# Performance work log

Hardware: AMD Instinct MI355X
Metric: run time of the kernel (lower is better)

## Reference

```python
import jax, jax.numpy as jnp
import numpy as np


def setup_inputs() -> dict:
    key = jax.random.key(0)
    ks = jax.random.split(key, 6)
    Q, S, D, C = 128, 512, 768, 64
    return {
        "query_reps": jax.random.normal(ks[0], (Q, D), dtype=jnp.float32),
        "support_reps": jax.random.normal(ks[1], (S, D), dtype=jnp.float32),
        "W1": jax.random.normal(ks[2], (2 * D, 2 * D), dtype=jnp.float32) * 0.02,
        "b1": jnp.zeros((2 * D,), dtype=jnp.float32),
        "W2": jax.random.normal(ks[3], (1, 2 * D), dtype=jnp.float32) * 0.02,
        "b2": jnp.zeros((1,), dtype=jnp.float32),
        "support_labels": jnp.sort(jax.random.randint(ks[4], (S,), 0, C)),
        "query_target_ids": jax.random.randint(ks[5], (Q,), 0, C),
        "num_classes": C,
    }


def reference(query_reps, support_reps, W1, b1, W2, b2,
              support_labels, query_target_ids, num_classes):
    D = query_reps.shape[1]
    # Original: concat_reps = cat([repeat_interleave(q, S), s.repeat(Q)], dim=1)
    # then relu(Linear_2Dx2D(concat)). Equivalent split-weight form avoids the
    # explicit [Q*S, 2D] concat: x @ W1.T = q @ W1[:, :D].T + s @ W1[:, D:].T
    hq = query_reps @ W1[:, :D].T        # [Q, 2D]
    hs = support_reps @ W1[:, D:].T      # [S, 2D]
    h = jax.nn.relu(hq[:, None, :] + hs[None, :, :] + b1)   # [Q, S, 2D]
    scores = jnp.einsum('qsd,d->qs', h, W2[0]) + b2[0]       # [Q, S]
    # aggregate_scores_by_label with support_reduction='score':
    # M one-hot [C, S] row-normalized (p=1) => per-label mean of scores.
    seg = jax.ops.segment_sum(scores.T, support_labels,
                              num_segments=num_classes).T     # [Q, C]
    counts = jax.ops.segment_sum(jnp.ones((support_labels.shape[0],), jnp.float32),
                                 support_labels, num_segments=num_classes)
    agg = seg / jnp.maximum(counts, 1.0)                      # [Q, C]
    logp = jax.nn.log_softmax(agg, axis=1)
    loss = -jnp.mean(jnp.take_along_axis(logp, query_target_ids[:, None], axis=1))
    preds = jnp.argmax(agg, axis=1)
    return (loss, preds == query_target_ids)
```

## Files before the change

kernel.cpp:

```cpp
#include <hip/hip_runtime.h>
#include <math.h>

#define QN 128
#define SN 512
#define DN 768
#define TDN 1536
#define CN 64
#define KSPLIT 2
#define KCH 384

#define HQP_ELEMS (KSPLIT * QN * TDN)
#define HSP_ELEMS (KSPLIT * SN * TDN)
#define ZERO_ELEMS (QN * CN)

typedef short short8 __attribute__((ext_vector_type(8)));
typedef float f32x4 __attribute__((ext_vector_type(4)));

#define LDS_STRIDE 40
#define PLANE (128 * LDS_STRIDE)

__device__ __forceinline__ short bf16_rtn(float x) {
    unsigned u = __float_as_uint(x);
    return (short)((u + 0x7fffu + ((u >> 16) & 1u)) >> 16);
}
__device__ __forceinline__ float bf16_tof(short s) {
    return __uint_as_float(((unsigned)(unsigned short)s) << 16);
}

__global__ __launch_bounds__(256) void gemm_kernel(
    const float* __restrict__ query, const float* __restrict__ support,
    const float* __restrict__ W1, float* __restrict__ hqp, float* __restrict__ hsp,
    float* __restrict__ zbuf, float* __restrict__ out)
{
    const int nt = blockIdx.x;
    const int mt = blockIdx.y;
    const int kz = blockIdx.z;
    const int tid = threadIdx.x;

    if (nt == 0 && kz == 0) {
        int o = (mt * 256 + tid) * 8;
        if (o < ZERO_ELEMS) {
            *(float4*)&zbuf[o]     = make_float4(0.f, 0.f, 0.f, 0.f);
            *(float4*)&zbuf[o + 4] = make_float4(0.f, 0.f, 0.f, 0.f);
        }
        if (mt == 0 && tid == 0) out[0] = 0.0f;
    }

    const float* A;
    float* Cout;
    int M0, Koff;
    if (mt == 0) { A = query;   M0 = 0;              Koff = 0;  Cout = hqp + (size_t)kz * QN * TDN; }
    else         { A = support; M0 = (mt - 1) * 128; Koff = DN; Cout = hsp + (size_t)kz * SN * TDN; }

    __shared__ short lds[2][4][PLANE];

    const int r  = tid >> 1;
    const int kh = (tid & 1) * 16;

    const float* Arow = &A [(size_t)(M0 + r) * DN  + kz * KCH + kh];
    const float* Brow = &W1[(size_t)(nt * 128 + r) * TDN + Koff + kz * KCH + kh];

    f32x4 acc[4][4];
    #pragma unroll
    for (int i = 0; i < 4; ++i)
        #pragma unroll
        for (int j = 0; j < 4; ++j)
            acc[i][j] = (f32x4){0.f, 0.f, 0.f, 0.f};

    auto stage = [&](short* plane, float4 v0, float4 v1, float4 v2, float4 v3) {
        float f[16] = {v0.x,v0.y,v0.z,v0.w, v1.x,v1.y,v1.z,v1.w,
                       v2.x,v2.y,v2.z,v2.w, v3.x,v3.y,v3.z,v3.w};
        short hi[16], lo[16];
        #pragma unroll
        for (int i = 0; i < 16; ++i) {
            hi[i] = bf16_rtn(f[i]);
            lo[i] = bf16_rtn(f[i] - bf16_tof(hi[i]));
        }
        short* dsth = plane + r * LDS_STRIDE + kh;
        #pragma unroll
        for (int i = 0; i < 16; ++i) dsth[i] = hi[i];
        short* dstl = plane + PLANE + r * LDS_STRIDE + kh;
        #pragma unroll
        for (int i = 0; i < 16; ++i) dstl[i] = lo[i];
    };

    {
        float4 a0 = *(const float4*)(Arow),     a1 = *(const float4*)(Arow + 4);
        float4 a2 = *(const float4*)(Arow + 8), a3 = *(const float4*)(Arow + 12);
        float4 b0 = *(const float4*)(Brow),     b1 = *(const float4*)(Brow + 4);
        float4 b2 = *(const float4*)(Brow + 8), b3 = *(const float4*)(Brow + 12);
        stage(lds[0][0], a0, a1, a2, a3);
        stage(lds[0][2], b0, b1, b2, b3);
    }
    __syncthreads();

    const int lane  = tid & 63;
    const int w     = tid >> 6;
    const int lm    = lane & 15;
    const int quad  = lane >> 4;
    const int wrow0 = (w >> 1) * 64;
    const int wcol0 = (w & 1) * 64;

    int buf = 0;
    for (int step = 0; step < 12; ++step) {
        float4 a0, a1, a2, a3, b0, b1, b2, b3;
        if (step < 11) {
            const float* An = Arow + (step + 1) * 32;
            const float* Bn = Brow + (step + 1) * 32;
            a0 = *(const float4*)(An);     a1 = *(const float4*)(An + 4);
            a2 = *(const float4*)(An + 8); a3 = *(const float4*)(An + 12);
            b0 = *(const float4*)(Bn);     b1 = *(const float4*)(Bn + 4);
            b2 = *(const float4*)(Bn + 8); b3 = *(const float4*)(Bn + 12);
        }

        const short* Ah = lds[buf][0];
        const short* Al = lds[buf][1];
        const short* Bh = lds[buf][2];
        const short* Bl = lds[buf][3];

        short8 ah[4], al[4], bh[4], bl[4];
        #pragma unroll
        for (int mi = 0; mi < 4; ++mi) {
            int off = (wrow0 + mi * 16 + lm) * LDS_STRIDE + quad * 8;
            ah[mi] = *(const short8*)&Ah[off];
            al[mi] = *(const short8*)&Al[off];
        }
        #pragma unroll
        for (int ni = 0; ni < 4; ++ni) {
            int off = (wcol0 + ni * 16 + lm) * LDS_STRIDE + quad * 8;
            bh[ni] = *(const short8*)&Bh[off];
            bl[ni] = *(const short8*)&Bl[off];
        }
        #pragma unroll
        for (int mi = 0; mi < 4; ++mi)
            #pragma unroll
            for (int ni = 0; ni < 4; ++ni) {
                acc[mi][ni] = __builtin_amdgcn_mfma_f32_16x16x32_bf16(ah[mi], bh[ni], acc[mi][ni], 0, 0, 0);
                acc[mi][ni] = __builtin_amdgcn_mfma_f32_16x16x32_bf16(ah[mi], bl[ni], acc[mi][ni], 0, 0, 0);
                acc[mi][ni] = __builtin_amdgcn_mfma_f32_16x16x32_bf16(al[mi], bh[ni], acc[mi][ni], 0, 0, 0);
            }

        if (step < 11) {
            int nb = buf ^ 1;
            stage(lds[nb][0], a0, a1, a2, a3);
            stage(lds[nb][2], b0, b1, b2, b3);
            __syncthreads();
            buf = nb;
        }
    }

    #pragma unroll
    for (int mi = 0; mi < 4; ++mi)
        #pragma unroll
        for (int ni = 0; ni < 4; ++ni) {
            int grow = M0 + wrow0 + mi * 16 + quad * 4;
            int gcol = nt * 128 + wcol0 + ni * 16 + lm;
            #pragma unroll
            for (int rr = 0; rr < 4; ++rr)
                Cout[(size_t)(grow + rr) * TDN + gcol] = acc[mi][ni][rr];
        }
}

#define JC 48
#define SSTR 68

__global__ __launch_bounds__(256) void score_kernel(
    const float* __restrict__ hqp, const float* __restrict__ hsp,
    const float* __restrict__ b1, const float* __restrict__ W2,
    const int* __restrict__ labels, float* __restrict__ aggbuf)
{
    const int jc = blockIdx.x;
    const int qt = blockIdx.y;
    const int st = blockIdx.z;

    __shared__ float hqL[64 * SSTR];
    __shared__ float hsL[64 * SSTR];
    __shared__ float w2s[JC];
    __shared__ int   lab[64];

    const int tid = threadIdx.x;
    if (tid < 64) lab[tid] = labels[st * 64 + tid];
    if (tid < 12) *(float4*)&w2s[tid * 4] = *(const float4*)&W2[jc * JC + tid * 4];

    #pragma unroll
    for (int l = 0; l < 6; ++l) {
        int idx  = tid + l * 256;
        int isHS = idx >= 768;
        int slot = isHS ? idx - 768 : idx;
        int row  = slot / 12;
        int q4   = slot - row * 12;
        int j    = jc * JC + q4 * 4;
        int phys = q4 ^ ((row >> 2) & 7);
        if (!isHS) {
            float4 h0 = *(const float4*)&hqp[(size_t)(qt * 64 + row) * TDN + j];
            float4 h1 = *(const float4*)&hqp[(size_t)QN * TDN + (size_t)(qt * 64 + row) * TDN + j];
            float4 bb = *(const float4*)&b1[j];
            *(float4*)&hqL[row * SSTR + phys * 4] =
                make_float4(h0.x + h1.x + bb.x, h0.y + h1.y + bb.y,
                            h0.z + h1.z + bb.z, h0.w + h1.w + bb.w);
        } else {
            float4 g0 = *(const float4*)&hsp[(size_t)(st * 64 + row) * TDN + j];
            float4 g1 = *(const float4*)&hsp[(size_t)SN * TDN + (size_t)(st * 64 + row) * TDN + j];
            *(float4*)&hsL[row * SSTR + phys * 4] =
                make_float4(g0.x + g1.x, g0.y + g1.y, g0.z + g1.z, g0.w + g1.w);
        }
    }
    __syncthreads();

    const int tx = tid & 15;
    const int ty = tid >> 4;
    float acc[4][4];
    #pragma unroll
    for (int i = 0; i < 4; ++i)
        #pragma unroll
        for (int j = 0; j < 4; ++j) acc[i][j] = 0.0f;

    const int akey = ty & 7;
    const int bkey = tx & 7;

    for (int jj4 = 0; jj4 < 12; ++jj4) {
        float4 a4[4], b4[4];
        const int pa = (jj4 ^ akey) * 4;
        const int pb = (jj4 ^ bkey) * 4;
        #pragma unroll
        for (int i = 0; i < 4; ++i)
            a4[i] = *(const float4*)&hqL[(ty * 4 + i) * SSTR + pa];
        #pragma unroll
        for (int j = 0; j < 4; ++j)
            b4[j] = *(const float4*)&hsL[(tx * 4 + j) * SSTR + pb];
        float4 w4 = *(const float4*)&w2s[jj4 * 4];

        #pragma unroll
        for (int c = 0; c < 4; ++c) {
            float w = (c == 0) ? w4.x : (c == 1) ? w4.y : (c == 2) ? w4.z : w4.w;
            float a[4] = { (c==0)?a4[0].x:(c==1)?a4[0].y:(c==2)?a4[0].z:a4[0].w,
                           (c==0)?a4[1].x:(c==1)?a4[1].y:(c==2)?a4[1].z:a4[1].w,
                           (c==0)?a4[2].x:(c==1)?a4[2].y:(c==2)?a4[2].z:a4[2].w,
                           (c==0)?a4[3].x:(c==1)?a4[3].y:(c==2)?a4[3].z:a4[3].w };
            float b[4] = { (c==0)?b4[0].x:(c==1)?b4[0].y:(c==2)?b4[0].z:b4[0].w,
                           (c==0)?b4[1].x:(c==1)?b4[1].y:(c==2)?b4[1].z:b4[1].w,
                           (c==0)?b4[2].x:(c==1)?b4[2].y:(c==2)?b4[2].z:b4[2].w,
                           (c==0)?b4[3].x:(c==1)?b4[3].y:(c==2)?b4[3].z:b4[3].w };
            #pragma unroll
            for (int i = 0; i < 4; ++i)
                #pragma unroll
                for (int j = 0; j < 4; ++j)
                    acc[i][j] += w * fmaxf(a[i] + b[j], 0.0f);
        }
    }

    {
        const int l0 = lab[tx * 4 + 0], l1 = lab[tx * 4 + 1];
        const int l2 = lab[tx * 4 + 2], l3 = lab[tx * 4 + 3];
        #pragma unroll
        for (int i = 0; i < 4; ++i) {
            float* aggrow = aggbuf + (size_t)(qt * 64 + ty * 4 + i) * CN;
            float runv = acc[i][0];
            int   runc = l0;
            if (l1 != runc) { atomicAdd(&aggrow[runc], runv); runv = 0.0f; runc = l1; }
            runv += acc[i][1];
            if (l2 != runc) { atomicAdd(&aggrow[runc], runv); runv = 0.0f; runc = l2; }
            runv += acc[i][2];
            if (l3 != runc) { atomicAdd(&aggrow[runc], runv); runv = 0.0f; runc = l3; }
            runv += acc[i][3];
            atomicAdd(&aggrow[runc], runv);
        }
    }
}

__global__ __launch_bounds__(256) void finale_kernel(
    const float* __restrict__ aggbuf, const int* __restrict__ labels,
    const int* __restrict__ tgt, float* __restrict__ out)
{
    __shared__ float cnt[CN];
    const int tid = threadIdx.x;
    if (tid < CN) cnt[tid] = 0.0f;
    __syncthreads();
    atomicAdd(&cnt[labels[tid]],       1.0f);
    atomicAdd(&cnt[labels[tid + 256]], 1.0f);
    __syncthreads();

    const int lane = tid & 63;
    const int q    = blockIdx.x * 4 + (tid >> 6);

    float v = aggbuf[(size_t)q * CN + lane] / fmaxf(cnt[lane], 1.0f);
    float av = v; int am = lane;
    #pragma unroll
    for (int off = 1; off < 64; off <<= 1) {
        float ov = __shfl_xor(av, off);
        int   oi = __shfl_xor(am, off);
        if (ov > av || (ov == av && oi < am)) { av = ov; am = oi; }
    }
    float m = av;
    float e = expf(v - m);
    #pragma unroll
    for (int off = 1; off < 64; off <<= 1)
        e += __shfl_xor(e, off);
    int t = tgt[q];
    float vt = __shfl(v, t, 64);
    if (lane == 0) {
        out[1 + q] = (am == t) ? 1.0f : 0.0f;
        atomicAdd(&out[0], -(vt - m - logf(e)) / (float)QN);
    }
}

extern "C" void kernel_launch(void* const* d_in, const int* in_sizes, int n_in,
                              void* d_out, int out_size, void* d_ws, size_t ws_size,
                              hipStream_t stream) {
    const float* query   = (const float*)d_in[0];
    const float* support = (const float*)d_in[1];
    const float* W1      = (const float*)d_in[2];
    const float* b1      = (const float*)d_in[3];
    const float* W2      = (const float*)d_in[4];
    const int* labels = (const int*)d_in[6];
    const int* tgt    = (const int*)d_in[7];

    float* ws     = (float*)d_ws;
    float* hqp    = ws;
    float* hsp    = hqp + HQP_ELEMS;
    float* aggbuf = hsp + HSP_ELEMS;
    float* out    = (float*)d_out;

    hipLaunchKernelGGL(gemm_kernel, dim3(12, 5, 2), dim3(256), 0, stream,
                       query, support, W1, hqp, hsp, aggbuf, out);
    hipLaunchKernelGGL(score_kernel, dim3(32, 2, 8), dim3(256), 0, stream,
                       hqp, hsp, b1, W2, labels, aggbuf);
    hipLaunchKernelGGL(finale_kernel, dim3(32), dim3(256), 0, stream,
                       aggbuf, labels, tgt, out);
}
```

Baseline: 139.2 us.

## Halve GEMM N-tile to double block count and stage scores in LDS for fewer atomics

```diff
diff --git a/kernel.cpp b/kernel.cpp
--- a/kernel.cpp
+++ b/kernel.cpp
@@ -16,8 +16,10 @@
 typedef short short8 __attribute__((ext_vector_type(8)));
 typedef float f32x4 __attribute__((ext_vector_type(4)));
 
-#define LDS_STRIDE 40
-#define PLANE (128 * LDS_STRIDE)
+#define ASTR 40
+#define APLANE (128 * ASTR)
+#define BPLANE (64 * ASTR)
+#define BUFSZ (2 * APLANE + 2 * BPLANE)
 
 __device__ __forceinline__ short bf16_rtn(float x) {
     unsigned u = __float_as_uint(x);
@@ -51,88 +53,95 @@
     int M0, Koff;
     if (mt == 0) { A = query;   M0 = 0;              Koff = 0;  Cout = hqp + (size_t)kz * QN * TDN; }
     else         { A = support; M0 = (mt - 1) * 128; Koff = DN; Cout = hsp + (size_t)kz * SN * TDN; }
-
-    __shared__ short lds[2][4][PLANE];
-
-    const int r  = tid >> 1;
-    const int kh = (tid & 1) * 16;
-
-    const float* Arow = &A [(size_t)(M0 + r) * DN  + kz * KCH + kh];
-    const float* Brow = &W1[(size_t)(nt * 128 + r) * TDN + Koff + kz * KCH + kh];
-
-    f32x4 acc[4][4];
-    #pragma unroll
-    for (int i = 0; i < 4; ++i)
+    const int N0 = nt * 64;
+
+    __shared__ short lds[2][BUFSZ];
+
+    const int ra  = tid >> 1;
+    const int kha = (tid & 1) * 16;
+    const int rb  = tid >> 2;
+    const int khb = (tid & 3) * 8;
+
+    const float* Arow = &A [(size_t)(M0 + ra) * DN  + kz * KCH + kha];
+    const float* Brow = &W1[(size_t)(N0 + rb) * TDN + Koff + kz * KCH + khb];
+
+    f32x4 acc[2][4];
+    #pragma unroll
+    for (int i = 0; i < 2; ++i)
         #pragma unroll
         for (int j = 0; j < 4; ++j)
             acc[i][j] = (f32x4){0.f, 0.f, 0.f, 0.f};
 
-    auto stage = [&](short* plane, float4 v0, float4 v1, float4 v2, float4 v3) {
+    auto stageA = [&](short* base, float4 v0, float4 v1, float4 v2, float4 v3) {
         float f[16] = {v0.x,v0.y,v0.z,v0.w, v1.x,v1.y,v1.z,v1.w,
                        v2.x,v2.y,v2.z,v2.w, v3.x,v3.y,v3.z,v3.w};
-        short hi[16], lo[16];
+        short* dh = base + ra * ASTR + kha;
+        short* dl = dh + APLANE;
         #pragma unroll
         for (int i = 0; i < 16; ++i) {
-            hi[i] = bf16_rtn(f[i]);
-            lo[i] = bf16_rtn(f[i] - bf16_tof(hi[i]));
-        }
-        short* dsth = plane + r * LDS_STRIDE + kh;
-        #pragma unroll
-        for (int i = 0; i < 16; ++i) dsth[i] = hi[i];
-        short* dstl = plane + PLANE + r * LDS_STRIDE + kh;
-        #pragma unroll
-        for (int i = 0; i < 16; ++i) dstl[i] = lo[i];
+            short h = bf16_rtn(f[i]);
+            dh[i] = h;
+            dl[i] = bf16_rtn(f[i] - bf16_tof(h));
+        }
+    };
+    auto stageB = [&](short* base, float4 v0, float4 v1) {
+        float f[8] = {v0.x,v0.y,v0.z,v0.w, v1.x,v1.y,v1.z,v1.w};
+        short* dh = base + 2 * APLANE + rb * ASTR + khb;
+        short* dl = dh + BPLANE;
+        #pragma unroll
+        for (int i = 0; i < 8; ++i) {
+            short h = bf16_rtn(f[i]);
+            dh[i] = h;
+            dl[i] = bf16_rtn(f[i] - bf16_tof(h));
+        }
     };
 
     {
         float4 a0 = *(const float4*)(Arow),     a1 = *(const float4*)(Arow + 4);
         float4 a2 = *(const float4*)(Arow + 8), a3 = *(const float4*)(Arow + 12);
         float4 b0 = *(const float4*)(Brow),     b1 = *(const float4*)(Brow + 4);
-        float4 b2 = *(const float4*)(Brow + 8), b3 = *(const float4*)(Brow + 12);
-        stage(lds[0][0], a0, a1, a2, a3);
-        stage(lds[0][2], b0, b1, b2, b3);
-    }
-    __syncthreads();
-
-    const int lane  = tid & 63;
-    const int w     = tid >> 6;
-    const int lm    = lane & 15;
-    const int quad  = lane >> 4;
-    const int wrow0 = (w >> 1) * 64;
-    const int wcol0 = (w & 1) * 64;
+        stageA(lds[0], a0, a1, a2, a3);
+        stageB(lds[0], b0, b1);
+    }
+    __syncthreads();
+
+    const int lane = tid & 63;
+    const int w    = tid >> 6;
+    const int lm   = lane & 15;
+    const int quad = lane >> 4;
+    const int wr0  = w * 32;
 
     int buf = 0;
     for (int step = 0; step < 12; ++step) {
-        float4 a0, a1, a2, a3, b0, b1, b2, b3;
+        float4 a0, a1, a2, a3, b0, b1;
         if (step < 11) {
             const float* An = Arow + (step + 1) * 32;
             const float* Bn = Brow + (step + 1) * 32;
             a0 = *(const float4*)(An);     a1 = *(const float4*)(An + 4);
             a2 = *(const float4*)(An + 8); a3 = *(const float4*)(An + 12);
             b0 = *(const float4*)(Bn);     b1 = *(const float4*)(Bn + 4);
-            b2 = *(const float4*)(Bn + 8); b3 = *(const float4*)(Bn + 12);
-        }
-
-        const short* Ah = lds[buf][0];
-        const short* Al = lds[buf][1];
-        const short* Bh = lds[buf][2];
-        const short* Bl = lds[buf][3];
-
-        short8 ah[4], al[4], bh[4], bl[4];
-        #pragma unroll
-        for (int mi = 0; mi < 4; ++mi) {
-            int off = (wrow0 + mi * 16 + lm) * LDS_STRIDE + quad * 8;
+        }
+
+        const short* Ah = lds[buf];
+        const short* Al = Ah + APLANE;
+        const short* Bh = Ah + 2 * APLANE;
+        const short* Bl = Bh + BPLANE;
+
+        short8 ah[2], al[2], bh[4], bl[4];
+        #pragma unroll
+        for (int mi = 0; mi < 2; ++mi) {
+            int off = (wr0 + mi * 16 + lm) * ASTR + quad * 8;
             ah[mi] = *(const short8*)&Ah[off];
             al[mi] = *(const short8*)&Al[off];
         }
         #pragma unroll
         for (int ni = 0; ni < 4; ++ni) {
-            int off = (wcol0 + ni * 16 + lm) * LDS_STRIDE + quad * 8;
+            int off = (ni * 16 + lm) * ASTR + quad * 8;
             bh[ni] = *(const short8*)&Bh[off];
             bl[ni] = *(const short8*)&Bl[off];
         }
         #pragma unroll
-        for (int mi = 0; mi < 4; ++mi)
+        for (int mi = 0; mi < 2; ++mi)
             #pragma unroll
             for (int ni = 0; ni < 4; ++ni) {
                 acc[mi][ni] = __builtin_amdgcn_mfma_f32_16x16x32_bf16(ah[mi], bh[ni], acc[mi][ni], 0, 0, 0);
@@ -142,19 +151,19 @@
 
         if (step < 11) {
             int nb = buf ^ 1;
-            stage(lds[nb][0], a0, a1, a2, a3);
-            stage(lds[nb][2], b0, b1, b2, b3);
+            stageA(lds[nb], a0, a1, a2, a3);
+            stageB(lds[nb], b0, b1);
             __syncthreads();
             buf = nb;
         }
     }
 
     #pragma unroll
-    for (int mi = 0; mi < 4; ++mi)
+    for (int mi = 0; mi < 2; ++mi)
         #pragma unroll
         for (int ni = 0; ni < 4; ++ni) {
-            int grow = M0 + wrow0 + mi * 16 + quad * 4;
-            int gcol = nt * 128 + wcol0 + ni * 16 + lm;
+            int grow = M0 + wr0 + mi * 16 + quad * 4;
+            int gcol = N0 + ni * 16 + lm;
             #pragma unroll
             for (int rr = 0; rr < 4; ++rr)
                 Cout[(size_t)(grow + rr) * TDN + gcol] = acc[mi][ni][rr];
@@ -175,6 +184,7 @@
 
     __shared__ float hqL[64 * SSTR];
     __shared__ float hsL[64 * SSTR];
+    __shared__ float sc[64 * SSTR];
     __shared__ float w2s[JC];
     __shared__ int   lab[64];
 
@@ -249,22 +259,26 @@
         }
     }
 
+    #pragma unroll
+    for (int i = 0; i < 4; ++i)
+        *(float4*)&sc[(ty * 4 + i) * SSTR + tx * 4] =
+            make_float4(acc[i][0], acc[i][1], acc[i][2], acc[i][3]);
+    __syncthreads();
+
     {
-        const int l0 = lab[tx * 4 + 0], l1 = lab[tx * 4 + 1];
-        const int l2 = lab[tx * 4 + 2], l3 = lab[tx * 4 + 3];
-        #pragma unroll
-        for (int i = 0; i < 4; ++i) {
-            float* aggrow = aggbuf + (size_t)(qt * 64 + ty * 4 + i) * CN;
-            float runv = acc[i][0];
-            int   runc = l0;
-            if (l1 != runc) { atomicAdd(&aggrow[runc], runv); runv = 0.0f; runc = l1; }
-            runv += acc[i][1];
-            if (l2 != runc) { atomicAdd(&aggrow[runc], runv); runv = 0.0f; runc = l2; }
-            runv += acc[i][2];
-            if (l3 != runc) { atomicAdd(&aggrow[runc], runv); runv = 0.0f; runc = l3; }
-            runv += acc[i][3];
-            atomicAdd(&aggrow[runc], runv);
-        }
+        int row = tid >> 2;
+        int seg = tid & 3;
+        float* aggrow = aggbuf + (size_t)(qt * 64 + row) * CN;
+        int   runc = lab[seg * 16];
+        float runv = 0.0f;
+        #pragma unroll
+        for (int k = 0; k < 16; ++k) {
+            int s = seg * 16 + k;
+            int c = lab[s];
+            if (c != runc) { atomicAdd(&aggrow[runc], runv); runv = 0.0f; runc = c; }
+            runv += sc[row * SSTR + s];
+        }
+        atomicAdd(&aggrow[runc], runv);
     }
 }
 
@@ -321,7 +335,7 @@
     float* aggbuf = hsp + HSP_ELEMS;
     float* out    = (float*)d_out;
 
-    hipLaunchKernelGGL(gemm_kernel, dim3(12, 5, 2), dim3(256), 0, stream,
+    hipLaunchKernelGGL(gemm_kernel, dim3(24, 5, 2), dim3(256), 0, stream,
                        query, support, W1, hqp, hsp, aggbuf, out);
     hipLaunchKernelGGL(score_kernel, dim3(32, 2, 8), dim3(256), 0, stream,
                        hqp, hsp, b1, W2, labels, aggbuf);
```

Result: faster. 123.7 us (-11.1%).
